# Performance work log

Measured on AMD Instinct MI355X. Metric: run time of the kernel, lower is better.

Reference implementation:

```python
import jax, jax.numpy as jnp
import numpy as np

B, S, D = 16, 2048, 400
HEADS, HEAD_SIZE = 4, 100
SCALE = 1.0 / np.float32(100.0 ** 0.5)


def setup_inputs() -> dict:
    key = jax.random.key(0)
    ks = jax.random.split(key, 8)
    return {
        "x": jax.random.normal(ks[0], (B, S, D), jnp.float32),
        "attn_kernel": jax.random.normal(ks[1], (3, D, HEAD_SIZE), jnp.float32) * 0.05,
        "attn_dense": jax.random.normal(ks[2], (D, HEADS * HEAD_SIZE), jnp.float32) * 0.05,
        "d1_w": jax.random.normal(ks[3], (400, 400), jnp.float32) * 0.05,
        "d1_b": jnp.zeros((400,), jnp.float32),
        "fc1_w": jax.random.normal(ks[4], (800, 512), jnp.float32) * 0.05,
        "fc1_b": jnp.zeros((512,), jnp.float32),
        "fc2_w": jax.random.normal(ks[5], (512, 256), jnp.float32) * 0.05,
        "fc2_b": jnp.zeros((256,), jnp.float32),
    }


def reference(x, attn_kernel, attn_dense, d1_w, d1_b, fc1_w, fc1_b, fc2_w, fc2_b):
    # Multi-head attention. NOTE: the original loops `heads` times over the SAME
    # shared kernel, so all 4 head outputs are identical; compute once, tile.
    WQ = jnp.einsum('bsd,dh->bsh', x, attn_kernel[0])  # [B,S,100]
    WK = jnp.einsum('bsd,dh->bsh', x, attn_kernel[1])
    WV = jnp.einsum('bsd,dh->bsh', x, attn_kernel[2])
    scores = jnp.einsum('bqh,bkh->bqk', WQ, WK) * SCALE  # [B,S,S]
    probs = jax.nn.softmax(scores, axis=-1)
    V = jnp.einsum('bqk,bkh->bqh', probs, WV)  # [B,S,100]
    out = jnp.tile(V, (1, 1, HEADS))  # concat of identical heads -> [B,S,400]
    out = jnp.einsum('bsd,de->bse', out, attn_dense)  # [B,S,400]
    # Dropout layers are identity at inference.
    h = jax.nn.relu(jnp.einsum('bsd,de->bse', out, d1_w) + d1_b)  # [B,S,400]
    pooled = jnp.concatenate([jnp.max(h, axis=1), jnp.mean(h, axis=1)], axis=-1)  # [B,800]
    h = jax.nn.relu(pooled @ fc1_w + fc1_b)  # [B,512]
    h = jax.nn.relu(h @ fc2_w + fc2_b)  # [B,256]
    return h
```

## Files before the change

kernel.cpp:

```cpp
#include <hip/hip_runtime.h>

typedef __attribute__((ext_vector_type(8))) _Float16 f16x8;
typedef __attribute__((ext_vector_type(4))) float f4v;
typedef __attribute__((ext_vector_type(8))) unsigned short us8;
typedef __attribute__((ext_vector_type(4))) unsigned short us4;
typedef unsigned short u16;

__device__ __forceinline__ u16 h2b(_Float16 h) { return __builtin_bit_cast(u16, h); }
__device__ __forceinline__ float b2f(u16 b) {
    return (float)__builtin_bit_cast(_Float16, b);
}

#define BAR() do { asm volatile("s_waitcnt lgkmcnt(0)" ::: "memory"); \
                   __builtin_amdgcn_s_barrier(); } while (0)

__global__ void k_w2p(const float* __restrict__ ad, const float* __restrict__ d1w,
                      float* __restrict__ w2p) {
    int i = blockIdx.x * 256 + threadIdx.x;
    if (i >= 51200) return;
    int es = blockIdx.y;
    int d = i / 400, j = i % 400;
    float acc = 0.f;
    if (d < 100) {
        const float* a0 = ad + d * 400 + es * 100;
        const float* wr = d1w + (es * 100) * 400 + j;
        #pragma unroll 4
        for (int e = 0; e < 100; ++e) {
            float av = a0[e] + a0[40000 + e] + a0[80000 + e] + a0[120000 + e];
            acc += av * wr[e * 400];
        }
    }
    w2p[es * 51200 + i] = acc;
}

__global__ void k_w2r(const float* __restrict__ w2p, u16* __restrict__ w2f) {
    int i = blockIdx.x * 256 + threadIdx.x;
    if (i >= 51200) return;
    float acc = w2p[i] + w2p[51200 + i] + w2p[102400 + i] + w2p[153600 + i];
    int d = i / 400, j = i % 400;
    int idx = ((j >> 4) * 4 + (d >> 5)) * 512 + (((d >> 3) & 3) * 16 + (j & 15)) * 8 + (d & 7);
    w2f[idx] = h2b((_Float16)acc);
}

__global__ void k_wprep(const float* __restrict__ ak, u16* __restrict__ wsp) {
    int i = blockIdx.x * 256 + threadIdx.x;
    if (i >= 159744) return;
    int k = i & 31, n = (i >> 5) & 127;
    int xx = i >> 12;
    int ks = xx % 13, m = xx / 13;
    int gk = ks * 32 + k;
    float v = (n < 100 && gk < 400) ? ak[m * 40000 + gk * 100 + n] : 0.f;
    _Float16 hb = (_Float16)v;
    _Float16 lb = (_Float16)(v - (float)hb);
    long base = (long)xx * 8192;
    int pos = n * 32 + ((((k >> 3) ^ (n & 3)) << 3) | (k & 7));
    wsp[base + pos] = h2b(hb);
    wsp[base + 4096 + pos] = h2b(lb);
}

__global__ __launch_bounds__(512) void k_gemm_qkv(
    const float* __restrict__ x, const u16* __restrict__ wsp,
    u16* __restrict__ QH, u16* __restrict__ KH, u16* __restrict__ VT) {
    __shared__ __align__(16) u16 smem[49152];

    const int tid = threadIdx.x;
    const int rowblk = blockIdx.x;
    const long row0 = (long)rowblk * 128;
    const int w = tid >> 6, l = tid & 63, g = l >> 4, c15 = l & 15;
    const int sr = tid >> 2, skc = tid & 3;

    f4v aQ[8], aK[8], aV[8];
    #pragma unroll
    for (int nt = 0; nt < 8; ++nt) {
        aQ[nt] = (f4v){0.f, 0.f, 0.f, 0.f};
        aK[nt] = (f4v){0.f, 0.f, 0.f, 0.f};
        aV[nt] = (f4v){0.f, 0.f, 0.f, 0.f};
    }

    const u16* wq  = wsp;
    const u16* wkh = wsp + 106496;
    const u16* wkl = wsp + 110592;
    const u16* wv  = wsp + 212992;

    float4 xr0, xr1;
    us8 wr[4];
    const int xpos = sr * 32 + ((skc * 8) ^ ((sr & 3) << 3));

    {
        const float* xp = x + (row0 + sr) * 400 + skc * 8;
        xr0 = *(const float4*)xp;
        xr1 = *(const float4*)(xp + 4);
        wr[0] = *(const us8*)&wq [(long)tid * 8];
        wr[1] = *(const us8*)&wkh[(long)tid * 8];
        wr[2] = *(const us8*)&wkl[(long)tid * 8];
        wr[3] = *(const us8*)&wv [(long)tid * 8];
        float va[8] = {xr0.x, xr0.y, xr0.z, xr0.w, xr1.x, xr1.y, xr1.z, xr1.w};
        us8 hi8, lo8;
        #pragma unroll
        for (int j = 0; j < 8; ++j) {
            _Float16 h = (_Float16)va[j];
            hi8[j] = h2b(h);
            lo8[j] = h2b((_Float16)(va[j] - (float)h));
        }
        *(us8*)&smem[xpos] = hi8;
        *(us8*)&smem[4096 + xpos] = lo8;
        *(us8*)&smem[8192  + tid * 8] = wr[0];
        *(us8*)&smem[12288 + tid * 8] = wr[1];
        *(us8*)&smem[16384 + tid * 8] = wr[2];
        *(us8*)&smem[20480 + tid * 8] = wr[3];
        const float* xp1 = x + (row0 + sr) * 400 + 32 + skc * 8;
        xr0 = *(const float4*)xp1;
        xr1 = *(const float4*)(xp1 + 4);
        wr[0] = *(const us8*)&wq [8192 + (long)tid * 8];
        wr[1] = *(const us8*)&wkh[8192 + (long)tid * 8];
        wr[2] = *(const us8*)&wkl[8192 + (long)tid * 8];
        wr[3] = *(const us8*)&wv [8192 + (long)tid * 8];
    }

    for (int ks = 0; ks < 13; ++ks) {
        BAR();
        u16* cb = smem + (ks & 1) * 24576;
        u16* sb = smem + ((ks & 1) ^ 1) * 24576;
        if (ks + 1 < 13) {
            float va[8] = {xr0.x, xr0.y, xr0.z, xr0.w, xr1.x, xr1.y, xr1.z, xr1.w};
            us8 hi8, lo8;
            #pragma unroll
            for (int j = 0; j < 8; ++j) {
                _Float16 h = (_Float16)va[j];
                hi8[j] = h2b(h);
                lo8[j] = h2b((_Float16)(va[j] - (float)h));
            }
            *(us8*)&sb[xpos] = hi8;
            *(us8*)&sb[4096 + xpos] = lo8;
            *(us8*)&sb[8192  + tid * 8] = wr[0];
            *(us8*)&sb[12288 + tid * 8] = wr[1];
            *(us8*)&sb[16384 + tid * 8] = wr[2];
            *(us8*)&sb[20480 + tid * 8] = wr[3];
            if (ks + 2 < 13) {
                if ((ks + 2) * 32 + skc * 8 < 400) {
                    const float* xp = x + (row0 + sr) * 400 + (ks + 2) * 32 + skc * 8;
                    xr0 = *(const float4*)xp;
                    xr1 = *(const float4*)(xp + 4);
                } else {
                    xr0 = make_float4(0.f, 0.f, 0.f, 0.f);
                    xr1 = make_float4(0.f, 0.f, 0.f, 0.f);
                }
                long wo = (long)(ks + 2) * 8192 + (long)tid * 8;
                wr[0] = *(const us8*)&wq [wo];
                wr[1] = *(const us8*)&wkh[wo];
                wr[2] = *(const us8*)&wkl[wo];
                wr[3] = *(const us8*)&wv [wo];
            }
        }
        const int arow = w * 16 + c15;
        const int axo = arow * 32 + ((g * 8) ^ ((arow & 3) << 3));
        f16x8 ah = *(const f16x8*)&cb[axo];
        f16x8 al = *(const f16x8*)&cb[4096 + axo];
        __builtin_amdgcn_s_setprio(1);
        #pragma unroll
        for (int nt = 0; nt < 8; ++nt) {
            int brow = nt * 16 + c15;
            int boff = brow * 32 + ((g * 8) ^ ((brow & 3) << 3));
            f16x8 qb = *(const f16x8*)&cb[8192 + boff];
            aQ[nt] = __builtin_amdgcn_mfma_f32_16x16x32_f16(ah, qb, aQ[nt], 0, 0, 0);
            aQ[nt] = __builtin_amdgcn_mfma_f32_16x16x32_f16(al, qb, aQ[nt], 0, 0, 0);
            f16x8 kh = *(const f16x8*)&cb[12288 + boff];
            aK[nt] = __builtin_amdgcn_mfma_f32_16x16x32_f16(ah, kh, aK[nt], 0, 0, 0);
            aK[nt] = __builtin_amdgcn_mfma_f32_16x16x32_f16(al, kh, aK[nt], 0, 0, 0);
            f16x8 kl = *(const f16x8*)&cb[16384 + boff];
            aK[nt] = __builtin_amdgcn_mfma_f32_16x16x32_f16(ah, kl, aK[nt], 0, 0, 0);
            f16x8 vb = *(const f16x8*)&cb[20480 + boff];
            aV[nt] = __builtin_amdgcn_mfma_f32_16x16x32_f16(ah, vb, aV[nt], 0, 0, 0);
            aV[nt] = __builtin_amdgcn_mfma_f32_16x16x32_f16(al, vb, aV[nt], 0, 0, 0);
        }
        __builtin_amdgcn_s_setprio(0);
    }
    BAR();
    u16* epi = smem;

    {
        const float qs = 0.14426950408889634f;
        #pragma unroll
        for (int nt = 0; nt < 8; ++nt) {
            #pragma unroll
            for (int r = 0; r < 4; ++r) {
                int row = w * 16 + 4 * g + r, col = nt * 16 + c15;
                epi[row * 128 + (col ^ ((row & 7) << 3))] =
                    h2b((_Float16)(aQ[nt][r] * qs));
            }
        }
        __syncthreads();
        #pragma unroll
        for (int r = 0; r < 4; ++r) {
            int u = tid + r * 512;
            int row = u >> 4, c = u & 15;
            *(us8*)&QH[(row0 + row) * 128 + c * 8] =
                *(const us8*)&epi[row * 128 + ((c * 8) ^ ((row & 7) << 3))];
        }
        __syncthreads();
    }
    {
        #pragma unroll
        for (int nt = 0; nt < 8; ++nt) {
            #pragma unroll
            for (int r = 0; r < 4; ++r) {
                int row = w * 16 + 4 * g + r, col = nt * 16 + c15;
                epi[row * 128 + (col ^ ((row & 7) << 3))] = h2b((_Float16)aK[nt][r]);
            }
        }
        __syncthreads();
        u16* dst = KH + (long)rowblk * 16384;
        #pragma unroll
        for (int r = 0; r < 4; ++r) {
            int u = tid + r * 512;
            *(us8*)&dst[(long)u * 8] = *(const us8*)&epi[u * 8];
        }
        __syncthreads();
    }
    {
        const int q0 = w * 16 + 4 * g;
        const int vtile = q0 >> 6, q0w = q0 & 63;
        #pragma unroll
        for (int nt = 0; nt < 8; ++nt) {
            int d = nt * 16 + c15;
            if (d < 112) {
                us4 v4;
                #pragma unroll
                for (int r = 0; r < 4; ++r) v4[r] = h2b((_Float16)aV[nt][r]);
                *(us4*)&epi[vtile * 8192 + d * 64 + (q0w ^ ((d & 7) << 3))] = v4;
            }
        }
        __syncthreads();
        #pragma unroll
        for (int r = 0; r < 4; ++r) {
            int u = tid + r * 512;
            int vt2 = u >> 10, uu = u & 1023;
            if (uu < 896)
                *(us8*)&VT[((long)(2 * rowblk + vt2)) * 8192 + (long)uu * 8] =
                    *(const us8*)&epi[u * 8];
        }
    }
}

__global__ __launch_bounds__(256) void k_flash(
    const u16* __restrict__ Qg, const u16* __restrict__ Kg,
    const u16* __restrict__ Vg, u16* __restrict__ VOI,
    float* __restrict__ ML) {
    __shared__ __align__(16) char KS[2][16384];
    __shared__ __align__(16) char VS[2][14336];
    __shared__ __align__(16) char PS[4][4096];

    const int tid = threadIdx.x;
    const int w = tid >> 6, l = tid & 63, g = l >> 4, c15 = l & 15;
    const int b = blockIdx.y, qt = blockIdx.x, half = blockIdx.z;
    const int t0 = half * 16;

    const u16* qp = Qg + ((long)b * 2048 + qt * 128 + w * 32 + c15) * 128;
    f16x8 qh[2][4];
    #pragma unroll
    for (int h = 0; h < 2; ++h)
        #pragma unroll
        for (int ks = 0; ks < 4; ++ks)
            qh[h][ks] = *(const f16x8*)(qp + h * 2048 + ks * 32 + g * 8);

    f4v O[2][7];
    #pragma unroll
    for (int h = 0; h < 2; ++h)
        #pragma unroll
        for (int i = 0; i < 7; ++i) O[h][i] = (f4v){0.f, 0.f, 0.f, 0.f};
    float lrow[2] = {0.f, 0.f};

    const u16* Kb = Kg + (long)b * 32 * 8192;
    const u16* Vb = Vg + (long)b * 32 * 8192;
    char* Pw = PS[w];

    us8 kreg[4], vreg[4];
    #pragma unroll
    for (int r = 0; r < 4; ++r) {
        int u = tid + r * 256;
        kreg[r] = *(const us8*)(Kb + (long)t0 * 8192 + (long)u * 8);
        if (u < 896) vreg[r] = *(const us8*)(Vb + (long)t0 * 8192 + (long)u * 8);
    }
    #pragma unroll
    for (int r = 0; r < 4; ++r) {
        int u = tid + r * 256;
        *(us8*)(KS[0] + u * 16) = kreg[r];
        if (u < 896) *(us8*)(VS[0] + u * 16) = vreg[r];
    }
    #pragma unroll
    for (int r = 0; r < 4; ++r) {
        int u = tid + r * 256;
        kreg[r] = *(const us8*)(Kb + (long)(t0 + 1) * 8192 + (long)u * 8);
        if (u < 896) vreg[r] = *(const us8*)(Vb + (long)(t0 + 1) * 8192 + (long)u * 8);
    }

    for (int t = t0; t < t0 + 16; ++t) {
        const int cur = (t - t0) & 1;
        BAR();
        if (t + 1 < t0 + 16) {
            #pragma unroll
            for (int r = 0; r < 4; ++r) {
                int u = tid + r * 256;
                *(us8*)(KS[cur ^ 1] + u * 16) = kreg[r];
                if (u < 896) *(us8*)(VS[cur ^ 1] + u * 16) = vreg[r];
            }
            if (t + 2 < t0 + 16) {
                #pragma unroll
                for (int r = 0; r < 4; ++r) {
                    int u = tid + r * 256;
                    kreg[r] = *(const us8*)(Kb + (long)(t + 2) * 8192 + (long)u * 8);
                    if (u < 896)
                        vreg[r] = *(const us8*)(Vb + (long)(t + 2) * 8192 + (long)u * 8);
                }
            }
        }
        const char* Kc = KS[cur];
        const char* Vc = VS[cur];

        f4v s[2][4];
        #pragma unroll
        for (int h = 0; h < 2; ++h)
            #pragma unroll
            for (int nt = 0; nt < 4; ++nt) s[h][nt] = (f4v){0.f, 0.f, 0.f, 0.f};
        __builtin_amdgcn_s_setprio(1);
        #pragma unroll
        for (int ks = 0; ks < 4; ++ks) {
            #pragma unroll
            for (int nt = 0; nt < 4; ++nt) {
                int key = nt * 16 + c15;
                f16x8 kf = *(const f16x8*)(Kc + key * 256 +
                                           ((ks * 64 + g * 16) ^ ((key & 7) << 4)));
                s[0][nt] = __builtin_amdgcn_mfma_f32_16x16x32_f16(kf, qh[0][ks], s[0][nt], 0, 0, 0);
                s[1][nt] = __builtin_amdgcn_mfma_f32_16x16x32_f16(kf, qh[1][ks], s[1][nt], 0, 0, 0);
            }
        }
        __builtin_amdgcn_s_setprio(0);

        #pragma unroll
        for (int h = 0; h < 2; ++h) {
            float sum = 0.f;
            #pragma unroll
            for (int nt = 0; nt < 4; ++nt) {
                #pragma unroll
                for (int r = 0; r < 4; ++r) {
                    float p = exp2f(s[h][nt][r]);
                    s[h][nt][r] = p;
                    sum += p;
                }
            }
            sum += __shfl_xor(sum, 16);
            sum += __shfl_xor(sum, 32);
            lrow[h] += sum;
        }

        #pragma unroll
        for (int h = 0; h < 2; ++h) {
            #pragma unroll
            for (int nt = 0; nt < 4; ++nt) {
                uint2 pw2;
                pw2.x = __builtin_bit_cast(unsigned int,
                            __builtin_amdgcn_cvt_pkrtz(s[h][nt][0], s[h][nt][1]));
                pw2.y = __builtin_bit_cast(unsigned int,
                            __builtin_amdgcn_cvt_pkrtz(s[h][nt][2], s[h][nt][3]));
                *(uint2*)(Pw + (h * 16 + c15) * 128 +
                          ((32 * nt + 8 * g) ^ ((c15 & 7) << 4))) = pw2;
            }
        }
        __builtin_amdgcn_s_setprio(1);
        #pragma unroll
        for (int k0 = 0; k0 < 2; ++k0) {
            f16x8 pa0 = *(const f16x8*)(Pw + c15 * 128 +
                                        ((k0 * 64 + g * 16) ^ ((c15 & 7) << 4)));
            f16x8 pa1 = *(const f16x8*)(Pw + (16 + c15) * 128 +
                                        ((k0 * 64 + g * 16) ^ ((c15 & 7) << 4)));
            #pragma unroll
            for (int dt = 0; dt < 7; ++dt) {
                int d = dt * 16 + c15;
                f16x8 vf = *(const f16x8*)(Vc + d * 128 +
                                           ((k0 * 64 + g * 16) ^ ((d & 7) << 4)));
                O[0][dt] = __builtin_amdgcn_mfma_f32_16x16x32_f16(pa0, vf, O[0][dt], 0, 0, 0);
                O[1][dt] = __builtin_amdgcn_mfma_f32_16x16x32_f16(pa1, vf, O[1][dt], 0, 0, 0);
            }
        }
        __builtin_amdgcn_s_setprio(0);
    }

    if (g == 0) {
        ((float*)Pw)[c15] = lrow[0];
        ((float*)Pw)[16 + c15] = lrow[1];
        ML[half * 32768 + b * 2048 + qt * 128 + w * 32 + c15] = lrow[0];
        ML[half * 32768 + b * 2048 + qt * 128 + w * 32 + 16 + c15] = lrow[1];
    }
    float linv[2][4];
    #pragma unroll
    for (int h = 0; h < 2; ++h)
        #pragma unroll
        for (int r = 0; r < 4; ++r)
            linv[h][r] = 1.f / ((float*)Pw)[h * 16 + 4 * g + r];
    u16* vout = VOI + (long)half * 4194304 + ((long)b * 16 + qt) * 16384;
    #pragma unroll
    for (int h = 0; h < 2; ++h) {
        #pragma unroll
        for (int r = 0; r < 4; ++r) {
            int rowl = w * 32 + h * 16 + 4 * g + r;
            int rsw = (4 * g + r) & 7;
            #pragma unroll
            for (int dt = 0; dt < 7; ++dt) {
                int d = dt * 16 + c15;
                int pos = rowl * 128 + ((((d >> 3) ^ rsw) << 3) | (d & 7));
                vout[pos] = h2b((_Float16)(O[h][dt][r] * linv[h][r]));
            }
        }
    }
}

__global__ __launch_bounds__(256) void k_hpool(
    const u16* __restrict__ VOI, const float* __restrict__ ML,
    const u16* __restrict__ W2F, const float* __restrict__ d1b,
    float* __restrict__ pmax, float* __restrict__ psum) {
    __shared__ __align__(16) u16 A[8192];
    __shared__ float redM[4][400], redS[4][400];
    __shared__ float wgt[64][2];
    const int tid = threadIdx.x;
    const int w = tid >> 6, l = tid & 63, g = l >> 4, c15 = l & 15;
    const int b = blockIdx.y, rt = blockIdx.x;

    if (tid < 64) {
        float a = ML[b * 2048 + rt * 64 + tid];
        float c = ML[32768 + b * 2048 + rt * 64 + tid];
        float inv = 1.f / (a + c);
        wgt[tid][0] = a * inv;
        wgt[tid][1] = c * inv;
    }
    __syncthreads();

    const u16* s1 = VOI + ((long)b * 32 + rt) * 8192;
    const u16* s2 = s1 + 4194304;
    #pragma unroll
    for (int r = 0; r < 4; ++r) {
        int u = tid + r * 256;
        int row = u >> 4;
        us8 p1 = *(const us8*)&s1[(long)u * 8];
        us8 p2 = *(const us8*)&s2[(long)u * 8];
        float w1 = wgt[row][0], w2 = wgt[row][1];
        us8 o;
        #pragma unroll
        for (int j = 0; j < 8; ++j)
            o[j] = h2b((_Float16)(w1 * b2f(p1[j]) + w2 * b2f(p2[j])));
        *(us8*)&A[u * 8] = o;
    }
    __syncthreads();

    const int arow = w * 16 + c15;
    f16x8 af[4];
    #pragma unroll
    for (int ks = 0; ks < 4; ++ks)
        af[ks] = *(const f16x8*)&A[arow * 128 + ((ks * 32 + g * 8) ^ ((arow & 7) << 3))];

    for (int nt = 0; nt < 25; ++nt) {
        f4v acc = (f4v){0.f, 0.f, 0.f, 0.f};
        #pragma unroll
        for (int ks = 0; ks < 4; ++ks) {
            f16x8 bf = *(const f16x8*)&W2F[(nt * 4 + ks) * 512 + l * 8];
            acc = __builtin_amdgcn_mfma_f32_16x16x32_f16(af[ks], bf, acc, 0, 0, 0);
        }
        float bias = d1b[nt * 16 + c15];
        float mx4 = -1e30f, sm4 = 0.f;
        #pragma unroll
        for (int r = 0; r < 4; ++r) {
            float h = fmaxf(acc[r] + bias, 0.f);
            mx4 = fmaxf(mx4, h);
            sm4 += h;
        }
        mx4 = fmaxf(mx4, __shfl_xor(mx4, 16));
        mx4 = fmaxf(mx4, __shfl_xor(mx4, 32));
        sm4 += __shfl_xor(sm4, 16);
        sm4 += __shfl_xor(sm4, 32);
        if (g == 0) {
            redM[w][nt * 16 + c15] = mx4;
            redS[w][nt * 16 + c15] = sm4;
        }
    }
    __syncthreads();
    for (int j = tid; j < 400; j += 256) {
        float mx = fmaxf(fmaxf(redM[0][j], redM[1][j]), fmaxf(redM[2][j], redM[3][j]));
        float sm = redS[0][j] + redS[1][j] + redS[2][j] + redS[3][j];
        pmax[((long)b * 32 + rt) * 400 + j] = mx;
        psum[((long)b * 32 + rt) * 400 + j] = sm;
    }
}

__global__ __launch_bounds__(256) void k_pred(
    const float* __restrict__ pmax, const float* __restrict__ psum,
    float* __restrict__ pooled) {
    __shared__ float rm[16][17], rs[16][17];
    const int b = blockIdx.x, jt = blockIdx.y, tid = threadIdx.x;
    const int jo = tid & 15, ts = tid >> 4;
    const int j = jt * 16 + jo;
    float mx = -1e30f, sm = 0.f;
    for (int t = ts; t < 32; t += 16) {
        mx = fmaxf(mx, pmax[((long)b * 32 + t) * 400 + j]);
        sm += psum[((long)b * 32 + t) * 400 + j];
    }
    rm[ts][jo] = mx; rs[ts][jo] = sm;
    __syncthreads();
    if (tid < 16) {
        float m2 = rm[0][tid], s2 = rs[0][tid];
        #pragma unroll
        for (int t = 1; t < 16; ++t) { m2 = fmaxf(m2, rm[t][tid]); s2 += rs[t][tid]; }
        pooled[b * 800 + jt * 16 + tid] = m2;
        pooled[b * 800 + 400 + jt * 16 + tid] = s2 * (1.f / 2048.f);
    }
}

__global__ __launch_bounds__(256) void k_fc1(
    const float* __restrict__ pooled, const float* __restrict__ w,
    const float* __restrict__ bias, float* __restrict__ out) {
    __shared__ float pl[800];
    __shared__ float red[16][17];
    const int b = blockIdx.x, jt = blockIdx.y, tid = threadIdx.x;
    const int jo = tid & 15, ks = tid >> 4;
    const int j = jt * 16 + jo;
    for (int i = tid; i < 800; i += 256) pl[i] = pooled[b * 800 + i];
    __syncthreads();
    float acc = 0.f;
    #pragma unroll 5
    for (int kk = 0; kk < 50; ++kk) {
        int k = ks * 50 + kk;
        acc += pl[k] * w[k * 512 + j];
    }
    red[ks][jo] = acc;
    __syncthreads();
    if (tid < 16) {
        float s = red[0][tid];
        #pragma unroll
        for (int t = 1; t < 16; ++t) s += red[t][tid];
        out[b * 512 + jt * 16 + tid] = fmaxf(s + bias[jt * 16 + tid], 0.f);
    }
}

__global__ __launch_bounds__(256) void k_fc2(
    const float* __restrict__ h, const float* __restrict__ w,
    const float* __restrict__ bias, float* __restrict__ out) {
    __shared__ float hl[512];
    __shared__ float red[16][17];
    const int b = blockIdx.x, jt = blockIdx.y, tid = threadIdx.x;
    const int jo = tid & 15, ks = tid >> 4;
    const int j = jt * 16 + jo;
    for (int i = tid; i < 512; i += 256) hl[i] = h[b * 512 + i];
    __syncthreads();
    float acc = 0.f;
    #pragma unroll 4
    for (int kk = 0; kk < 32; ++kk) {
        int k = ks * 32 + kk;
        acc += hl[k] * w[k * 256 + j];
    }
    red[ks][jo] = acc;
    __syncthreads();
    if (tid < 16) {
        float s = red[0][tid];
        #pragma unroll
        for (int t = 1; t < 16; ++t) s += red[t][tid];
        out[b * 256 + jt * 16 + tid] = fmaxf(s + bias[jt * 16 + tid], 0.f);
    }
}

extern "C" void kernel_launch(void* const* d_in, const int* in_sizes, int n_in,
                              void* d_out, int out_size, void* d_ws, size_t ws_size,
                              hipStream_t stream) {
    const float* x          = (const float*)d_in[0];
    const float* attn_kernel= (const float*)d_in[1];
    const float* attn_dense = (const float*)d_in[2];
    const float* d1_w       = (const float*)d_in[3];
    const float* d1_b       = (const float*)d_in[4];
    const float* fc1_w      = (const float*)d_in[5];
    const float* fc1_b      = (const float*)d_in[6];
    const float* fc2_w      = (const float*)d_in[7];
    const float* fc2_b      = (const float*)d_in[8];
    float* out = (float*)d_out;
    char*  wsb = (char*)d_ws;

    u16*    QH   = (u16*)(wsb);
    u16*    KH   = (u16*)(wsb + 8388608);
    u16*    VT   = (u16*)(wsb + 16777216);
    u16*    VOI  = (u16*)(wsb + 25165824);
    u16*    WSP  = (u16*)(wsb + 41943040);
    u16*    W2F  = (u16*)(wsb + 42582016);
    float*  PMAX = (float*)(wsb + 42844416);
    float*  PSUM = (float*)(wsb + 43663616);
    float*  ML   = (float*)(wsb + 44566784);
    float*  W2P  = (float*)(wsb + 44828928);
    float*  POOL = (float*)(wsb + 45648128);
    float*  FC1  = (float*)(wsb + 45699328);

    k_wprep<<<624, 256, 0, stream>>>(attn_kernel, WSP);
    k_w2p <<<dim3(200, 4), 256, 0, stream>>>(attn_dense, d1_w, W2P);
    k_w2r <<<200, 256, 0, stream>>>(W2P, W2F);
    k_gemm_qkv<<<256, 512, 0, stream>>>(x, WSP, QH, KH, VT);
    k_flash<<<dim3(16, 16, 2), 256, 0, stream>>>(QH, KH, VT, VOI, ML);
    k_hpool<<<dim3(32, 16), 256, 0, stream>>>(VOI, ML, W2F, d1_b, PMAX, PSUM);
    k_pred<<<dim3(16, 25), 256, 0, stream>>>(PMAX, PSUM, POOL);
    k_fc1 <<<dim3(16, 32), 256, 0, stream>>>(POOL, fc1_w, fc1_b, FC1);
    k_fc2 <<<dim3(16, 16), 256, 0, stream>>>(FC1, fc2_w, fc2_b, out);
}
```

Baseline: 137.1 us.

## Split flash key tiles across two wave groups and compact V/output layouts

The flash kernel grows from 256 to 512 threads. Each group of four waves now handles half the keys of every 64-key tile, and the two partial O accumulators and row sums are reduced through shared memory at the end. V^T and the intermediate attention output are stored with a compact 112-wide stride instead of padded 128, which reduces global traffic, and the pooling kernel zero-fills the padding columns itself. This doubles the waves per block to hide latency, at the cost of an extra LDS reduction, more barrier participants and a larger shared-memory footprint that may lower block occupancy.

```diff
diff --git a/kernel.cpp b/kernel.cpp
--- a/kernel.cpp
+++ b/kernel.cpp
@@ -236,26 +236,25 @@
             int u = tid + r * 512;
             int vt2 = u >> 10, uu = u & 1023;
             if (uu < 896)
-                *(us8*)&VT[((long)(2 * rowblk + vt2)) * 8192 + (long)uu * 8] =
+                *(us8*)&VT[((long)(2 * rowblk + vt2)) * 7168 + (long)uu * 8] =
                     *(const us8*)&epi[u * 8];
         }
     }
 }
 
-__global__ __launch_bounds__(256) void k_flash(
+__global__ __launch_bounds__(512, 4) void k_flash(
     const u16* __restrict__ Qg, const u16* __restrict__ Kg,
     const u16* __restrict__ Vg, u16* __restrict__ VOI,
     float* __restrict__ ML) {
-    __shared__ __align__(16) char KS[2][16384];
-    __shared__ __align__(16) char VS[2][14336];
-    __shared__ __align__(16) char PS[4][4096];
+    __shared__ __align__(16) char smem[77824];
 
     const int tid = threadIdx.x;
-    const int w = tid >> 6, l = tid & 63, g = l >> 4, c15 = l & 15;
+    const int w = tid >> 6, l = tid & 63, g = (l >> 4) & 3, c15 = l & 15;
+    const int qg = w & 3, kh = w >> 2;
     const int b = blockIdx.y, qt = blockIdx.x, half = blockIdx.z;
     const int t0 = half * 16;
 
-    const u16* qp = Qg + ((long)b * 2048 + qt * 128 + w * 32 + c15) * 128;
+    const u16* qp = Qg + ((long)b * 2048 + qt * 128 + qg * 32 + c15) * 128;
     f16x8 qh[2][4];
     #pragma unroll
     for (int h = 0; h < 2; ++h)
@@ -271,27 +270,27 @@
     float lrow[2] = {0.f, 0.f};
 
     const u16* Kb = Kg + (long)b * 32 * 8192;
-    const u16* Vb = Vg + (long)b * 32 * 8192;
-    char* Pw = PS[w];
-
-    us8 kreg[4], vreg[4];
-    #pragma unroll
-    for (int r = 0; r < 4; ++r) {
-        int u = tid + r * 256;
+    const u16* Vb = Vg + (long)b * 32 * 7168;
+    char* Pw = smem + 61440 + w * 2048;
+
+    us8 kreg[2], vreg[2];
+    #pragma unroll
+    for (int r = 0; r < 2; ++r) {
+        int u = tid + r * 512;
         kreg[r] = *(const us8*)(Kb + (long)t0 * 8192 + (long)u * 8);
-        if (u < 896) vreg[r] = *(const us8*)(Vb + (long)t0 * 8192 + (long)u * 8);
-    }
-    #pragma unroll
-    for (int r = 0; r < 4; ++r) {
-        int u = tid + r * 256;
-        *(us8*)(KS[0] + u * 16) = kreg[r];
-        if (u < 896) *(us8*)(VS[0] + u * 16) = vreg[r];
-    }
-    #pragma unroll
-    for (int r = 0; r < 4; ++r) {
-        int u = tid + r * 256;
+        if (u < 896) vreg[r] = *(const us8*)(Vb + (long)t0 * 7168 + (long)u * 8);
+    }
+    #pragma unroll
+    for (int r = 0; r < 2; ++r) {
+        int u = tid + r * 512;
+        *(us8*)(smem + u * 16) = kreg[r];
+        if (u < 896) *(us8*)(smem + 32768 + u * 16) = vreg[r];
+    }
+    #pragma unroll
+    for (int r = 0; r < 2; ++r) {
+        int u = tid + r * 512;
         kreg[r] = *(const us8*)(Kb + (long)(t0 + 1) * 8192 + (long)u * 8);
-        if (u < 896) vreg[r] = *(const us8*)(Vb + (long)(t0 + 1) * 8192 + (long)u * 8);
+        if (u < 896) vreg[r] = *(const us8*)(Vb + (long)(t0 + 1) * 7168 + (long)u * 8);
     }
 
     for (int t = t0; t < t0 + 16; ++t) {
@@ -299,35 +298,36 @@
         BAR();
         if (t + 1 < t0 + 16) {
             #pragma unroll
-            for (int r = 0; r < 4; ++r) {
-                int u = tid + r * 256;
-                *(us8*)(KS[cur ^ 1] + u * 16) = kreg[r];
-                if (u < 896) *(us8*)(VS[cur ^ 1] + u * 16) = vreg[r];
+            for (int r = 0; r < 2; ++r) {
+                int u = tid + r * 512;
+                *(us8*)(smem + (cur ^ 1) * 16384 + u * 16) = kreg[r];
+                if (u < 896)
+                    *(us8*)(smem + 32768 + (cur ^ 1) * 14336 + u * 16) = vreg[r];
             }
             if (t + 2 < t0 + 16) {
                 #pragma unroll
-                for (int r = 0; r < 4; ++r) {
-                    int u = tid + r * 256;
+                for (int r = 0; r < 2; ++r) {
+                    int u = tid + r * 512;
                     kreg[r] = *(const us8*)(Kb + (long)(t + 2) * 8192 + (long)u * 8);
                     if (u < 896)
-                        vreg[r] = *(const us8*)(Vb + (long)(t + 2) * 8192 + (long)u * 8);
+                        vreg[r] = *(const us8*)(Vb + (long)(t + 2) * 7168 + (long)u * 8);
                 }
             }
         }
-        const char* Kc = KS[cur];
-        const char* Vc = VS[cur];
-
-        f4v s[2][4];
+        const char* Kc = smem + cur * 16384;
+        const char* Vc = smem + 32768 + cur * 14336;
+
+        f4v s[2][2];
         #pragma unroll
         for (int h = 0; h < 2; ++h)
             #pragma unroll
-            for (int nt = 0; nt < 4; ++nt) s[h][nt] = (f4v){0.f, 0.f, 0.f, 0.f};
+            for (int nt = 0; nt < 2; ++nt) s[h][nt] = (f4v){0.f, 0.f, 0.f, 0.f};
         __builtin_amdgcn_s_setprio(1);
         #pragma unroll
         for (int ks = 0; ks < 4; ++ks) {
             #pragma unroll
-            for (int nt = 0; nt < 4; ++nt) {
-                int key = nt * 16 + c15;
+            for (int nt = 0; nt < 2; ++nt) {
+                int key = kh * 32 + nt * 16 + c15;
                 f16x8 kf = *(const f16x8*)(Kc + key * 256 +
                                            ((ks * 64 + g * 16) ^ ((key & 7) << 4)));
                 s[0][nt] = __builtin_amdgcn_mfma_f32_16x16x32_f16(kf, qh[0][ks], s[0][nt], 0, 0, 0);
@@ -340,7 +340,7 @@
         for (int h = 0; h < 2; ++h) {
             float sum = 0.f;
             #pragma unroll
-            for (int nt = 0; nt < 4; ++nt) {
+            for (int nt = 0; nt < 2; ++nt) {
                 #pragma unroll
                 for (int r = 0; r < 4; ++r) {
                     float p = exp2f(s[h][nt][r]);
@@ -356,59 +356,71 @@
         #pragma unroll
         for (int h = 0; h < 2; ++h) {
             #pragma unroll
-            for (int nt = 0; nt < 4; ++nt) {
+            for (int nt = 0; nt < 2; ++nt) {
                 uint2 pw2;
                 pw2.x = __builtin_bit_cast(unsigned int,
                             __builtin_amdgcn_cvt_pkrtz(s[h][nt][0], s[h][nt][1]));
                 pw2.y = __builtin_bit_cast(unsigned int,
                             __builtin_amdgcn_cvt_pkrtz(s[h][nt][2], s[h][nt][3]));
-                *(uint2*)(Pw + (h * 16 + c15) * 128 +
-                          ((32 * nt + 8 * g) ^ ((c15 & 7) << 4))) = pw2;
+                *(uint2*)(Pw + h * 1024 + c15 * 64 +
+                          ((nt * 32 + g * 8) ^ ((c15 & 3) << 4))) = pw2;
             }
         }
         __builtin_amdgcn_s_setprio(1);
-        #pragma unroll
-        for (int k0 = 0; k0 < 2; ++k0) {
-            f16x8 pa0 = *(const f16x8*)(Pw + c15 * 128 +
-                                        ((k0 * 64 + g * 16) ^ ((c15 & 7) << 4)));
-            f16x8 pa1 = *(const f16x8*)(Pw + (16 + c15) * 128 +
-                                        ((k0 * 64 + g * 16) ^ ((c15 & 7) << 4)));
-            #pragma unroll
-            for (int dt = 0; dt < 7; ++dt) {
-                int d = dt * 16 + c15;
-                f16x8 vf = *(const f16x8*)(Vc + d * 128 +
-                                           ((k0 * 64 + g * 16) ^ ((d & 7) << 4)));
-                O[0][dt] = __builtin_amdgcn_mfma_f32_16x16x32_f16(pa0, vf, O[0][dt], 0, 0, 0);
-                O[1][dt] = __builtin_amdgcn_mfma_f32_16x16x32_f16(pa1, vf, O[1][dt], 0, 0, 0);
-            }
+        f16x8 pa0 = *(const f16x8*)(Pw + c15 * 64 + ((g * 16) ^ ((c15 & 3) << 4)));
+        f16x8 pa1 = *(const f16x8*)(Pw + 1024 + c15 * 64 + ((g * 16) ^ ((c15 & 3) << 4)));
+        #pragma unroll
+        for (int dt = 0; dt < 7; ++dt) {
+            int d = dt * 16 + c15;
+            f16x8 vf = *(const f16x8*)(Vc + d * 128 +
+                                       ((kh * 64 + g * 16) ^ ((d & 7) << 4)));
+            O[0][dt] = __builtin_amdgcn_mfma_f32_16x16x32_f16(pa0, vf, O[0][dt], 0, 0, 0);
+            O[1][dt] = __builtin_amdgcn_mfma_f32_16x16x32_f16(pa1, vf, O[1][dt], 0, 0, 0);
         }
         __builtin_amdgcn_s_setprio(0);
     }
 
-    if (g == 0) {
-        ((float*)Pw)[c15] = lrow[0];
-        ((float*)Pw)[16 + c15] = lrow[1];
-        ML[half * 32768 + b * 2048 + qt * 128 + w * 32 + c15] = lrow[0];
-        ML[half * 32768 + b * 2048 + qt * 128 + w * 32 + 16 + c15] = lrow[1];
-    }
-    float linv[2][4];
-    #pragma unroll
-    for (int h = 0; h < 2; ++h)
-        #pragma unroll
-        for (int r = 0; r < 4; ++r)
-            linv[h][r] = 1.f / ((float*)Pw)[h * 16 + 4 * g + r];
-    u16* vout = VOI + (long)half * 4194304 + ((long)b * 16 + qt) * 16384;
-    #pragma unroll
-    for (int h = 0; h < 2; ++h) {
-        #pragma unroll
-        for (int r = 0; r < 4; ++r) {
-            int rowl = w * 32 + h * 16 + 4 * g + r;
-            int rsw = (4 * g + r) & 7;
-            #pragma unroll
-            for (int dt = 0; dt < 7; ++dt) {
-                int d = dt * 16 + c15;
-                int pos = rowl * 128 + ((((d >> 3) ^ rsw) << 3) | (d & 7));
-                vout[pos] = h2b((_Float16)(O[h][dt][r] * linv[h][r]));
+    float* PSf = (float*)Pw;
+    if (g == 0) { PSf[c15] = lrow[0]; PSf[16 + c15] = lrow[1]; }
+    BAR();
+    if (kh == 1) {
+        char* ex = smem + qg * 14336;
+        #pragma unroll
+        for (int h = 0; h < 2; ++h)
+            #pragma unroll
+            for (int dt = 0; dt < 7; ++dt)
+                *(f4v*)(ex + ((h * 7 + dt) * 64 + l) * 16) = O[h][dt];
+    }
+    BAR();
+    if (kh == 0) {
+        const char* ex = smem + qg * 14336;
+        #pragma unroll
+        for (int h = 0; h < 2; ++h)
+            #pragma unroll
+            for (int dt = 0; dt < 7; ++dt)
+                O[h][dt] += *(const f4v*)(ex + ((h * 7 + dt) * 64 + l) * 16);
+        const float* PSp = (const float*)(smem + 61440 + (w + 4) * 2048);
+        float linv[2][4];
+        #pragma unroll
+        for (int h = 0; h < 2; ++h)
+            #pragma unroll
+            for (int r = 0; r < 4; ++r)
+                linv[h][r] = 1.f / (PSf[h * 16 + 4 * g + r] + PSp[h * 16 + 4 * g + r]);
+        if (g == 0) {
+            long mbase = (long)half * 32768 + b * 2048 + qt * 128 + qg * 32;
+            ML[mbase + c15]      = PSf[c15] + PSp[c15];
+            ML[mbase + 16 + c15] = PSf[16 + c15] + PSp[16 + c15];
+        }
+        u16* vout = VOI + ((long)(half * 16 + b) * 2048 + qt * 128 + qg * 32) * 112;
+        #pragma unroll
+        for (int h = 0; h < 2; ++h) {
+            #pragma unroll
+            for (int r = 0; r < 4; ++r) {
+                int row = h * 16 + 4 * g + r;
+                #pragma unroll
+                for (int dt = 0; dt < 7; ++dt)
+                    vout[row * 112 + dt * 16 + c15] =
+                        h2b((_Float16)(O[h][dt][r] * linv[h][r]));
             }
         }
     }
@@ -432,22 +444,29 @@
         wgt[tid][0] = a * inv;
         wgt[tid][1] = c * inv;
     }
-    __syncthreads();
-
-    const u16* s1 = VOI + ((long)b * 32 + rt) * 8192;
-    const u16* s2 = s1 + 4194304;
+    if (tid < 128) {
+        int r = tid >> 1, c = 14 + (tid & 1);
+        us8 z = {0, 0, 0, 0, 0, 0, 0, 0};
+        *(us8*)&A[r * 128 + ((c * 8) ^ ((r & 7) << 3))] = z;
+    }
+    __syncthreads();
+
+    const u16* s1 = VOI + ((long)b * 2048 + rt * 64) * 112;
+    const u16* s2 = VOI + ((long)(16 + b) * 2048 + rt * 64) * 112;
     #pragma unroll
     for (int r = 0; r < 4; ++r) {
         int u = tid + r * 256;
-        int row = u >> 4;
-        us8 p1 = *(const us8*)&s1[(long)u * 8];
-        us8 p2 = *(const us8*)&s2[(long)u * 8];
-        float w1 = wgt[row][0], w2 = wgt[row][1];
-        us8 o;
-        #pragma unroll
-        for (int j = 0; j < 8; ++j)
-            o[j] = h2b((_Float16)(w1 * b2f(p1[j]) + w2 * b2f(p2[j])));
-        *(us8*)&A[u * 8] = o;
+        if (u < 896) {
+            int row = u / 14, c = u % 14;
+            us8 p1 = *(const us8*)&s1[row * 112 + c * 8];
+            us8 p2 = *(const us8*)&s2[row * 112 + c * 8];
+            float w1 = wgt[row][0], w2 = wgt[row][1];
+            us8 o;
+            #pragma unroll
+            for (int j = 0; j < 8; ++j)
+                o[j] = h2b((_Float16)(w1 * b2f(p1[j]) + w2 * b2f(p2[j])));
+            *(us8*)&A[row * 128 + ((c * 8) ^ ((row & 7) << 3))] = o;
+        }
     }
     __syncthreads();
 
@@ -583,21 +602,21 @@
     u16*    QH   = (u16*)(wsb);
     u16*    KH   = (u16*)(wsb + 8388608);
     u16*    VT   = (u16*)(wsb + 16777216);
-    u16*    VOI  = (u16*)(wsb + 25165824);
-    u16*    WSP  = (u16*)(wsb + 41943040);
-    u16*    W2F  = (u16*)(wsb + 42582016);
-    float*  PMAX = (float*)(wsb + 42844416);
-    float*  PSUM = (float*)(wsb + 43663616);
-    float*  ML   = (float*)(wsb + 44566784);
-    float*  W2P  = (float*)(wsb + 44828928);
-    float*  POOL = (float*)(wsb + 45648128);
-    float*  FC1  = (float*)(wsb + 45699328);
+    u16*    VOI  = (u16*)(wsb + 24117248);
+    u16*    WSP  = (u16*)(wsb + 38797312);
+    u16*    W2F  = (u16*)(wsb + 39436288);
+    float*  PMAX = (float*)(wsb + 39538688);
+    float*  PSUM = (float*)(wsb + 40357888);
+    float*  ML   = (float*)(wsb + 41177088);
+    float*  W2P  = (float*)(wsb + 41439232);
+    float*  POOL = (float*)(wsb + 42258432);
+    float*  FC1  = (float*)(wsb + 42309632);
 
     k_wprep<<<624, 256, 0, stream>>>(attn_kernel, WSP);
     k_w2p <<<dim3(200, 4), 256, 0, stream>>>(attn_dense, d1_w, W2P);
     k_w2r <<<200, 256, 0, stream>>>(W2P, W2F);
     k_gemm_qkv<<<256, 512, 0, stream>>>(x, WSP, QH, KH, VT);
-    k_flash<<<dim3(16, 16, 2), 256, 0, stream>>>(QH, KH, VT, VOI, ML);
+    k_flash<<<dim3(16, 16, 2), 512, 0, stream>>>(QH, KH, VT, VOI, ML);
     k_hpool<<<dim3(32, 16), 256, 0, stream>>>(VOI, ML, W2F, d1_b, PMAX, PSUM);
     k_pred<<<dim3(16, 25), 256, 0, stream>>>(PMAX, PSUM, POOL);
     k_fc1 <<<dim3(16, 32), 256, 0, stream>>>(POOL, fc1_w, fc1_b, FC1);
```

Measured after the change: 195.5 us. 42.6% more time.
